# Kernel optimization log

Measured on AMD Instinct MI355X. Metric: run time of the kernel, lower is better.

The kernel has to match this reference:

```python
import jax, jax.numpy as jnp
import numpy as np

N_EMBD = 1024
B, T = 4, 2048

def setup_inputs() -> dict:
    key = jax.random.key(0)
    k1, k2, k3, k4 = jax.random.split(key, 4)
    s = 1.0 / np.sqrt(N_EMBD)
    return {
        "x": jax.random.normal(k1, (B, T, N_EMBD), dtype=jnp.float32),
        "Wq": jax.random.normal(k2, (N_EMBD, N_EMBD), dtype=jnp.float32) * s,
        "Wk": jax.random.normal(k3, (N_EMBD, N_EMBD), dtype=jnp.float32) * s,
        "Wv": jax.random.normal(k4, (N_EMBD, N_EMBD), dtype=jnp.float32) * s,
    }

def reference(x, Wq, Wk, Wv):
    # x: [B,T,C]; torch Linear (no bias): y = x @ W.T
    Bq, Tq, C = x.shape
    q = jnp.einsum('btc,dc->btd', x, Wq)
    k = jnp.einsum('btc,dc->btd', x, Wk)
    v = jnp.einsum('btc,dc->btd', x, Wv)
    att = jnp.einsum('bqd,bkd->bqk', q, k) / jnp.sqrt(jnp.float32(C))
    causal = jnp.tril(jnp.ones((Tq, Tq), dtype=bool))  # [T,T]
    att = jnp.where(causal, att, -jnp.inf)
    w = jax.nn.softmax(att, axis=-1)
    # dropout is identity in eval mode
    out = jnp.einsum('bqk,bkd->bqd', w, v)
    return out
```

## Files before the change

kernel.cpp:

```cpp
#include <hip/hip_runtime.h>
#include <stdint.h>

typedef __attribute__((ext_vector_type(8))) __bf16 bf16x8;
typedef __attribute__((ext_vector_type(8))) unsigned short ushort8;
typedef __attribute__((ext_vector_type(4))) float f32x4;

static __device__ __forceinline__ unsigned short f2bf(float f) {
  unsigned u = __float_as_uint(f);
  u += 0x7fffu + ((u >> 16) & 1u);
  return (unsigned short)(u >> 16);
}

union U16cast { ushort8 u; bf16x8 b; };
static __device__ __forceinline__ bf16x8 as_bf16x8(ushort8 x) { U16cast t; t.u = x; return t.b; }
static __device__ __forceinline__ bf16x8 ldfrag(const unsigned short* p) {
  return as_bf16x8(*(const ushort8*)p);
}

#define GLD_LDS16(g, l)                                                        \
  __builtin_amdgcn_global_load_lds(                                            \
      (const __attribute__((address_space(1))) void*)(g),                      \
      (__attribute__((address_space(3))) void*)(l), 16, 0, 0)

__global__ __launch_bounds__(256) void cast_all(
    const float* __restrict__ x, const float* __restrict__ Wq,
    const float* __restrict__ Wk, const float* __restrict__ Wv,
    unsigned short* __restrict__ out, float* __restrict__ lzero,
    long nx4, long nw4, long n4) {
  long g = (long)blockIdx.x * blockDim.x + threadIdx.x;
  if (g < 2048) ((float4*)lzero)[g] = (float4){0.f, 0.f, 0.f, 0.f};
  long i = g;
  long stride = (long)gridDim.x * blockDim.x;
  for (; i < n4; i += stride) {
    const float4* src;
    long j = i;
    if (j < nx4) {
      src = (const float4*)x;
    } else {
      j -= nx4;
      if (j < nw4) src = (const float4*)Wq;
      else if (j < 2 * nw4) { src = (const float4*)Wk; j -= nw4; }
      else { src = (const float4*)Wv; j -= 2 * nw4; }
    }
    float4 v = src[j];
    ushort4 o;
    o.x = f2bf(v.x); o.y = f2bf(v.y); o.z = f2bf(v.z); o.w = f2bf(v.w);
    *(ushort4*)(out + i * 4) = o;
  }
}

__global__ __launch_bounds__(512, 4) void gemm_qkv(
    const unsigned short* __restrict__ A, const unsigned short* __restrict__ B,
    unsigned short* __restrict__ qkv, unsigned short* __restrict__ vT) {
  __shared__ __align__(16) unsigned short As[3][4096];
  __shared__ __align__(16) unsigned short Bs[3][8192];

  int wg = blockIdx.x;
  wg = (wg & 7) * 96 + (wg >> 3);
  const int bm = wg / 12, bn = wg % 12;
  const int m0 = bm << 7, n0 = bn << 8;

  const int tid = threadIdx.x;

  const int srow = tid >> 2;
  const int sseg = (tid & 3) ^ ((srow >> 1) & 3);
  const unsigned short* sa = A + (long)(m0 + srow) * 1024 + sseg * 8;
  const unsigned short* sb0 = B + (long)(n0 + srow) * 1024 + sseg * 8;
  const unsigned short* sb1 = sb0 + (long)128 * 1024;
  unsigned short* dA = &As[0][0] + tid * 8;
  unsigned short* dB = &Bs[0][0] + tid * 8;

#define STG_SA(kt, s)  GLD_LDS16(sa + (kt) * 32, dA + (s) * 4096)
#define STG_SB0(kt, s) GLD_LDS16(sb0 + (kt) * 32, dB + (s) * 8192)
#define STG_SB1(kt, s) GLD_LDS16(sb1 + (kt) * 32, dB + (s) * 8192 + 4096)

  const int lane = tid & 63;
  const int w = tid >> 6;
  const int wr = w >> 2;
  const int wc = w & 3;
  const int fr = lane & 15;
  const int kb = lane >> 4;
  const int segr = (kb ^ ((fr >> 1) & 3)) << 3;
  const unsigned short* rA = &As[0][0] + (wr * 64 + fr) * 32 + segr;
  const unsigned short* rB = &Bs[0][0] + (wc * 64 + fr) * 32 + segr;

  f32x4 acc[4][4];
#pragma unroll
  for (int mf = 0; mf < 4; ++mf)
#pragma unroll
    for (int nf = 0; nf < 4; ++nf)
      acc[mf][nf] = (f32x4){0.f, 0.f, 0.f, 0.f};

  STG_SA(0, 0); STG_SB0(0, 0); STG_SB1(0, 0);
  STG_SA(1, 1); STG_SB0(1, 1); STG_SB1(1, 1);
  asm volatile("s_waitcnt vmcnt(3)" ::: "memory");
  __builtin_amdgcn_s_barrier();
  __builtin_amdgcn_sched_barrier(0);

  int c0 = 0, c2 = 2;
#pragma unroll 1
  for (int kt = 0; kt < 32; ++kt) {
    const unsigned short* pA = rA + c0 * 4096;
    const unsigned short* pB = rB + c0 * 8192;
    bf16x8 av[4], bv0, bv1, bv2, bv3;

#pragma unroll
    for (int mf = 0; mf < 4; ++mf) av[mf] = ldfrag(pA + mf * 512);
    bv0 = ldfrag(pB);
    bv1 = ldfrag(pB + 512);
    if (kt < 30) {
      STG_SA(kt + 2, c2);
      STG_SB0(kt + 2, c2);
      asm volatile("s_waitcnt vmcnt(3)" ::: "memory");
    } else {
      asm volatile("s_waitcnt vmcnt(0)" ::: "memory");
    }
    __builtin_amdgcn_s_barrier();
    asm volatile("s_waitcnt lgkmcnt(0)" ::: "memory");
    __builtin_amdgcn_sched_barrier(0);
    __builtin_amdgcn_s_setprio(1);
#pragma unroll
    for (int mf = 0; mf < 4; ++mf) {
      acc[mf][0] = __builtin_amdgcn_mfma_f32_16x16x32_bf16(av[mf], bv0, acc[mf][0], 0, 0, 0);
      acc[mf][1] = __builtin_amdgcn_mfma_f32_16x16x32_bf16(av[mf], bv1, acc[mf][1], 0, 0, 0);
    }
    __builtin_amdgcn_s_setprio(0);
    __builtin_amdgcn_s_barrier();
    __builtin_amdgcn_sched_barrier(0);

    bv2 = ldfrag(pB + 1024);
    bv3 = ldfrag(pB + 1536);
    if (kt < 30) {
      STG_SB1(kt + 2, c2);
      asm volatile("s_waitcnt vmcnt(3)" ::: "memory");
    } else {
      asm volatile("s_waitcnt vmcnt(0)" ::: "memory");
    }
    __builtin_amdgcn_s_barrier();
    asm volatile("s_waitcnt lgkmcnt(0)" ::: "memory");
    __builtin_amdgcn_sched_barrier(0);
    __builtin_amdgcn_s_setprio(1);
#pragma unroll
    for (int mf = 0; mf < 4; ++mf) {
      acc[mf][2] = __builtin_amdgcn_mfma_f32_16x16x32_bf16(av[mf], bv2, acc[mf][2], 0, 0, 0);
      acc[mf][3] = __builtin_amdgcn_mfma_f32_16x16x32_bf16(av[mf], bv3, acc[mf][3], 0, 0, 0);
    }
    __builtin_amdgcn_s_setprio(0);
    __builtin_amdgcn_s_barrier();
    __builtin_amdgcn_sched_barrier(0);

    c0 = (c0 == 2) ? 0 : c0 + 1;
    c2 = (c2 == 2) ? 0 : c2 + 1;
  }
#undef STG_SA
#undef STG_SB0
#undef STG_SB1

  const int rq = kb << 2;
  if (n0 < 2048) {
#pragma unroll
    for (int mf = 0; mf < 4; ++mf) {
      const int row = m0 + wr * 64 + mf * 16 + rq;
#pragma unroll
      for (int nf = 0; nf < 4; ++nf) {
        const int col = n0 + wc * 64 + nf * 16 + fr;
#pragma unroll
        for (int r = 0; r < 4; ++r)
          qkv[(long)(row + r) * 3072 + col] = f2bf(acc[mf][nf][r]);
      }
    }
  } else {
    const int b2 = m0 >> 11;
    const int t0 = (m0 & 2047) + wr * 64;
#pragma unroll
    for (int mf = 0; mf < 4; ++mf) {
      const int trow = t0 + mf * 16 + rq;
#pragma unroll
      for (int nf = 0; nf < 4; ++nf) {
        const int colv = (n0 - 2048) + wc * 64 + nf * 16 + fr;
        ushort4 o;
        o.x = f2bf(acc[mf][nf][0]); o.y = f2bf(acc[mf][nf][1]);
        o.z = f2bf(acc[mf][nf][2]); o.w = f2bf(acc[mf][nf][3]);
        *(ushort4*)(vT + ((long)b2 * 1024 + colv) * 2048 + trow) = o;
      }
    }
  }
}

template <int MODE>
__global__ __launch_bounds__(256, 4) void gemm128(
    const unsigned short* __restrict__ A, const unsigned short* __restrict__ Bp,
    void* __restrict__ Cout, float* __restrict__ lbuf) {
  __shared__ __align__(16) unsigned short As[2][4096];
  __shared__ __align__(16) unsigned short Bs[2][4096];

  constexpr int LDA = (MODE == 1) ? 3072 : 2048;

  const int wgid = blockIdx.x;
  int m0, n0, b;
  if constexpr (MODE == 1) {
    b = wgid & 3;
    const int t = wgid >> 2;
    int bm = 0;
    while ((bm + 2) * (bm + 1) / 2 <= t) ++bm;
    const int bn = t - bm * (bm + 1) / 2;
    m0 = bm << 7; n0 = bn << 7;
  } else {
    const int xcd = wgid & 7;
    const int inner = wgid >> 3;
    const int s = inner >> 5;
    const int rem = inner & 31;
    b = rem >> 3;
    const int bn = rem & 7;
    const int bm = s ? (15 - xcd) : xcd;
    m0 = bm << 7; n0 = bn << 7;
  }

  const unsigned short* Ab = A;
  const unsigned short* Bb = Bp;
  if constexpr (MODE == 1) {
    Ab += (long)b * 2048 * 3072;
    Bb += (long)b * 2048 * 3072;
  } else {
    Ab += (long)b * 2048 * 2048;
    Bb += (long)b * 1024 * 2048;
  }

  const int tid = threadIdx.x;

  const int srow = tid >> 2;
  const int sseg = (tid & 3) ^ ((srow >> 1) & 3);
  const unsigned short* sa = Ab + (long)(m0 + srow) * LDA + sseg * 8;
  const unsigned short* sb = Bb + (long)(n0 + srow) * LDA + sseg * 8;
  const long sRj = (long)64 * LDA;
  unsigned short* dA = &As[0][0] + tid * 8;
  unsigned short* dB = &Bs[0][0] + tid * 8;

#define STG(kt, s)                                                             \
  do {                                                                         \
    GLD_LDS16(sa + (kt) * 32, dA + (s) * 4096);                                \
    GLD_LDS16(sa + sRj + (kt) * 32, dA + (s) * 4096 + 2048);                   \
    GLD_LDS16(sb + (kt) * 32, dB + (s) * 4096);                                \
    GLD_LDS16(sb + sRj + (kt) * 32, dB + (s) * 4096 + 2048);                   \
  } while (0)

  const int lane = tid & 63;
  const int w = tid >> 6;
  const int wr = w >> 1;
  const int wc = w & 1;
  const int fr = lane & 15;
  const int kb = lane >> 4;
  const unsigned short* rA0 = &As[0][0] + wr * 64 * 32;
  const unsigned short* rB0 = &Bs[0][0] + wc * 64 * 32;

  f32x4 acc[4][4];
#pragma unroll
  for (int mf = 0; mf < 4; ++mf)
#pragma unroll
    for (int nf = 0; nf < 4; ++nf)
      acc[mf][nf] = (f32x4){0.f, 0.f, 0.f, 0.f};

  const int kend = (MODE == 2) ? (m0 + 128) : 1024;
  const int NT = kend >> 5;

  STG(0, 0);
  __syncthreads();

  for (int kt = 0; kt < NT; ++kt) {
    const int s = kt & 1;
    if (kt + 1 < NT) STG(kt + 1, s ^ 1);

    bf16x8 av[4], bvv[4];
#pragma unroll
    for (int mf = 0; mf < 4; ++mf) {
      const int row = mf * 16 + fr;
      const int segr = (kb ^ ((row >> 1) & 3)) << 3;
      av[mf] = ldfrag(rA0 + s * 4096 + row * 32 + segr);
    }
#pragma unroll
    for (int nf = 0; nf < 4; ++nf) {
      const int row = nf * 16 + fr;
      const int segr = (kb ^ ((row >> 1) & 3)) << 3;
      bvv[nf] = ldfrag(rB0 + s * 4096 + row * 32 + segr);
    }

#pragma unroll
    for (int mf = 0; mf < 4; ++mf)
#pragma unroll
      for (int nf = 0; nf < 4; ++nf)
        acc[mf][nf] = __builtin_amdgcn_mfma_f32_16x16x32_bf16(av[mf], bvv[nf], acc[mf][nf], 0, 0, 0);

    __syncthreads();
  }
#undef STG

  const int rq = kb << 2;
  if constexpr (MODE == 1) {
    unsigned short* Pu = (unsigned short*)Cout + (long)b * 2048 * 2048;
    float* lrow = lbuf + b * 2048;
#pragma unroll
    for (int mf = 0; mf < 4; ++mf) {
      const int row = m0 + wr * 64 + mf * 16 + rq;
      float psum0 = 0.f, psum1 = 0.f, psum2 = 0.f, psum3 = 0.f;
#pragma unroll
      for (int nf = 0; nf < 4; ++nf) {
        const int col = n0 + wc * 64 + nf * 16 + fr;
        float e0 = (col > row + 0) ? 0.f : __expf(acc[mf][nf][0] * 0.03125f);
        float e1 = (col > row + 1) ? 0.f : __expf(acc[mf][nf][1] * 0.03125f);
        float e2 = (col > row + 2) ? 0.f : __expf(acc[mf][nf][2] * 0.03125f);
        float e3 = (col > row + 3) ? 0.f : __expf(acc[mf][nf][3] * 0.03125f);
        psum0 += e0; psum1 += e1; psum2 += e2; psum3 += e3;
        Pu[(long)(row + 0) * 2048 + col] = f2bf(e0);
        Pu[(long)(row + 1) * 2048 + col] = f2bf(e1);
        Pu[(long)(row + 2) * 2048 + col] = f2bf(e2);
        Pu[(long)(row + 3) * 2048 + col] = f2bf(e3);
      }
#pragma unroll
      for (int off = 1; off < 16; off <<= 1) {
        psum0 += __shfl_xor(psum0, off);
        psum1 += __shfl_xor(psum1, off);
        psum2 += __shfl_xor(psum2, off);
        psum3 += __shfl_xor(psum3, off);
      }
      if (fr == 0) {
        atomicAdd(&lrow[row + 0], psum0);
        atomicAdd(&lrow[row + 1], psum1);
        atomicAdd(&lrow[row + 2], psum2);
        atomicAdd(&lrow[row + 3], psum3);
      }
    }
  } else {
    float* Cf = (float*)Cout + (long)b * 2048 * 1024;
    const float* lrow = lbuf + b * 2048;
#pragma unroll
    for (int mf = 0; mf < 4; ++mf) {
      const int row = m0 + wr * 64 + mf * 16 + rq;
      float il0 = 1.0f / lrow[row + 0];
      float il1 = 1.0f / lrow[row + 1];
      float il2 = 1.0f / lrow[row + 2];
      float il3 = 1.0f / lrow[row + 3];
#pragma unroll
      for (int nf = 0; nf < 4; ++nf) {
        const int col = n0 + wc * 64 + nf * 16 + fr;
        Cf[(long)(row + 0) * 1024 + col] = acc[mf][nf][0] * il0;
        Cf[(long)(row + 1) * 1024 + col] = acc[mf][nf][1] * il1;
        Cf[(long)(row + 2) * 1024 + col] = acc[mf][nf][2] * il2;
        Cf[(long)(row + 3) * 1024 + col] = acc[mf][nf][3] * il3;
      }
    }
  }
}

extern "C" void kernel_launch(void* const* d_in, const int* in_sizes, int n_in,
                              void* d_out, int out_size, void* d_ws, size_t ws_size,
                              hipStream_t stream) {
  const float* x  = (const float*)d_in[0];
  const float* Wq = (const float*)d_in[1];
  const float* Wk = (const float*)d_in[2];
  const float* Wv = (const float*)d_in[3];
  float* out = (float*)d_out;

  const int Bb = 4, T = 2048, C = 1024;
  const long BT = (long)Bb * T;
  const int N3 = 3 * C;

  char* ws = (char*)d_ws;
  unsigned short* xb   = (unsigned short*)ws; ws += BT * C * 2;
  unsigned short* wbuf = (unsigned short*)ws; ws += (long)N3 * C * 2;
  unsigned short* qkv  = (unsigned short*)ws; ws += BT * N3 * 2;
  unsigned short* vT   = (unsigned short*)ws; ws += BT * C * 2;
  unsigned short* Pu   = (unsigned short*)ws; ws += (long)Bb * T * T * 2;
  float* lbuf          = (float*)ws;          ws += BT * 4;

  const long nx4 = BT * C / 4, nw4 = (long)C * C / 4;
  cast_all<<<2048, 256, 0, stream>>>(x, Wq, Wk, Wv, xb, lbuf, nx4, nw4, nx4 + 3 * nw4);

  gemm_qkv<<<dim3(768, 1, 1), 512, 0, stream>>>(xb, wbuf, qkv, vT);

  gemm128<1><<<dim3(544, 1, 1), 256, 0, stream>>>(qkv, qkv + C, Pu, lbuf);

  gemm128<2><<<dim3(512, 1, 1), 256, 0, stream>>>(Pu, vT, out, lbuf);
}
```

Before: 157.5 us.

## Enlarge QKV GEMM tile to 256x256 with BK=64 double-buffered pipeline

The QKV projection GEMM now uses 256x256 output tiles with a K-step of 64 instead of 128x256 tiles with K-step 32, and a two-stage double buffer replaces the three-stage buffer. Each of the eight waves computes a 128x64 subtile in four interleaved phases, issuing global-to-LDS loads between MFMA phases. The grid is halved and the block swizzle is updated. The aim is more reuse per loaded byte and fewer barriers per FLOP. The cost is more LDS and registers, so occupancy drops to two blocks per CU, and 384 blocks leave a partial wave on the CUs.

```diff
diff --git a/kernel.cpp b/kernel.cpp
--- a/kernel.cpp
+++ b/kernel.cpp
@@ -16,6 +16,8 @@
 static __device__ __forceinline__ bf16x8 ldfrag(const unsigned short* p) {
   return as_bf16x8(*(const ushort8*)p);
 }
+
+#define MFMA16(a, b, c) __builtin_amdgcn_mfma_f32_16x16x32_bf16((a), (b), (c), 0, 0, 0)
 
 #define GLD_LDS16(g, l)                                                        \
   __builtin_amdgcn_global_load_lds(                                            \
@@ -49,30 +51,27 @@
   }
 }
 
-__global__ __launch_bounds__(512, 4) void gemm_qkv(
+__global__ __launch_bounds__(512, 2) void gemm_qkv(
     const unsigned short* __restrict__ A, const unsigned short* __restrict__ B,
     unsigned short* __restrict__ qkv, unsigned short* __restrict__ vT) {
-  __shared__ __align__(16) unsigned short As[3][4096];
-  __shared__ __align__(16) unsigned short Bs[3][8192];
+  __shared__ __align__(16) unsigned short As[2][16384];
+  __shared__ __align__(16) unsigned short Bs[2][16384];
 
   int wg = blockIdx.x;
-  wg = (wg & 7) * 96 + (wg >> 3);
+  wg = (wg & 7) * 48 + (wg >> 3);
   const int bm = wg / 12, bn = wg % 12;
-  const int m0 = bm << 7, n0 = bn << 8;
+  const int m0 = bm << 8, n0 = bn << 8;
 
   const int tid = threadIdx.x;
-
-  const int srow = tid >> 2;
-  const int sseg = (tid & 3) ^ ((srow >> 1) & 3);
-  const unsigned short* sa = A + (long)(m0 + srow) * 1024 + sseg * 8;
-  const unsigned short* sb0 = B + (long)(n0 + srow) * 1024 + sseg * 8;
-  const unsigned short* sb1 = sb0 + (long)128 * 1024;
-  unsigned short* dA = &As[0][0] + tid * 8;
-  unsigned short* dB = &Bs[0][0] + tid * 8;
-
-#define STG_SA(kt, s)  GLD_LDS16(sa + (kt) * 32, dA + (s) * 4096)
-#define STG_SB0(kt, s) GLD_LDS16(sb0 + (kt) * 32, dB + (s) * 8192)
-#define STG_SB1(kt, s) GLD_LDS16(sb1 + (kt) * 32, dB + (s) * 8192 + 4096)
+  const int sq = tid >> 3;
+  const int gseg = (tid & 7) ^ (sq & 7);
+  const unsigned short* pAg = A + (long)(m0 + sq) * 1024 + gseg * 8;
+  const unsigned short* pBg = B + (long)(n0 + sq) * 1024 + gseg * 8;
+  unsigned short* dAl = &As[0][0] + tid * 8;
+  unsigned short* dBl = &Bs[0][0] + tid * 8;
+
+#define SA(q, kt, bo) GLD_LDS16(pAg + (q) * 65536 + (kt) * 64, dAl + (bo) + (q) * 4096)
+#define SB(q, kt, bo) GLD_LDS16(pBg + (q) * 65536 + (kt) * 64, dBl + (bo) + (q) * 4096)
 
   const int lane = tid & 63;
   const int w = tid >> 6;
@@ -80,107 +79,147 @@
   const int wc = w & 3;
   const int fr = lane & 15;
   const int kb = lane >> 4;
-  const int segr = (kb ^ ((fr >> 1) & 3)) << 3;
-  const unsigned short* rA = &As[0][0] + (wr * 64 + fr) * 32 + segr;
-  const unsigned short* rB = &Bs[0][0] + (wc * 64 + fr) * 32 + segr;
-
-  f32x4 acc[4][4];
-#pragma unroll
-  for (int mf = 0; mf < 4; ++mf)
+  const int f7 = fr & 7;
+  const int s0 = (kb ^ f7) << 3;
+  const int s1 = s0 ^ 32;
+  const unsigned short* rA = &As[0][0] + (wr * 128 + fr) * 64;
+  const unsigned short* rB = &Bs[0][0] + (wc * 64 + fr) * 64;
+
+  f32x4 acc[8][4];
+#pragma unroll
+  for (int mf = 0; mf < 8; ++mf)
 #pragma unroll
     for (int nf = 0; nf < 4; ++nf)
       acc[mf][nf] = (f32x4){0.f, 0.f, 0.f, 0.f};
 
-  STG_SA(0, 0); STG_SB0(0, 0); STG_SB1(0, 0);
-  STG_SA(1, 1); STG_SB0(1, 1); STG_SB1(1, 1);
-  asm volatile("s_waitcnt vmcnt(3)" ::: "memory");
-  __builtin_amdgcn_s_barrier();
-  __builtin_amdgcn_sched_barrier(0);
-
-  int c0 = 0, c2 = 2;
+  bf16x8 av[4][2], b0[2][2], b1[2][2];
+
+  SB(0, 0, 0); SB(1, 0, 0); SB(2, 0, 0); SB(3, 0, 0);
+  SA(0, 0, 0); SA(2, 0, 0); SA(1, 0, 0); SA(3, 0, 0);
+
 #pragma unroll 1
-  for (int kt = 0; kt < 32; ++kt) {
-    const unsigned short* pA = rA + c0 * 4096;
-    const unsigned short* pB = rB + c0 * 8192;
-    bf16x8 av[4], bv0, bv1, bv2, bv3;
-
-#pragma unroll
-    for (int mf = 0; mf < 4; ++mf) av[mf] = ldfrag(pA + mf * 512);
-    bv0 = ldfrag(pB);
-    bv1 = ldfrag(pB + 512);
-    if (kt < 30) {
-      STG_SA(kt + 2, c2);
-      STG_SB0(kt + 2, c2);
-      asm volatile("s_waitcnt vmcnt(3)" ::: "memory");
-    } else {
-      asm volatile("s_waitcnt vmcnt(0)" ::: "memory");
-    }
-    __builtin_amdgcn_s_barrier();
+  for (int t = 0; t < 16; ++t) {
+    const int bo = (t & 1) << 14;
+    const int bo1 = bo ^ 16384;
+    const int k1 = t + 1;
+    const bool nl = (t < 15);
+    const unsigned short* pa = rA + bo;
+    const unsigned short* pb = rB + bo;
+
+    if (nl) { SB(0, k1, bo1); SB(1, k1, bo1); }
+    if (nl) asm volatile("s_waitcnt vmcnt(4)" ::: "memory");
+    else    asm volatile("s_waitcnt vmcnt(2)" ::: "memory");
+    __builtin_amdgcn_s_barrier();
+    __builtin_amdgcn_sched_barrier(0);
+#pragma unroll
+    for (int mf = 0; mf < 4; ++mf) {
+      av[mf][0] = ldfrag(pa + mf * 1024 + s0);
+      av[mf][1] = ldfrag(pa + mf * 1024 + s1);
+    }
+#pragma unroll
+    for (int nf = 0; nf < 2; ++nf) {
+      b0[nf][0] = ldfrag(pb + nf * 1024 + s0);
+      b0[nf][1] = ldfrag(pb + nf * 1024 + s1);
+    }
     asm volatile("s_waitcnt lgkmcnt(0)" ::: "memory");
     __builtin_amdgcn_sched_barrier(0);
     __builtin_amdgcn_s_setprio(1);
 #pragma unroll
+    for (int mf = 0; mf < 4; ++mf)
+#pragma unroll
+      for (int nf = 0; nf < 2; ++nf) {
+        acc[mf][nf] = MFMA16(av[mf][0], b0[nf][0], acc[mf][nf]);
+        acc[mf][nf] = MFMA16(av[mf][1], b0[nf][1], acc[mf][nf]);
+      }
+    __builtin_amdgcn_s_setprio(0);
+    __builtin_amdgcn_s_barrier();
+
+    if (nl) { SB(2, k1, bo1); SB(3, k1, bo1); }
+    __builtin_amdgcn_s_barrier();
+    __builtin_amdgcn_sched_barrier(0);
+#pragma unroll
+    for (int nf = 0; nf < 2; ++nf) {
+      b1[nf][0] = ldfrag(pb + 2048 + nf * 1024 + s0);
+      b1[nf][1] = ldfrag(pb + 2048 + nf * 1024 + s1);
+    }
+    asm volatile("s_waitcnt lgkmcnt(0)" ::: "memory");
+    __builtin_amdgcn_sched_barrier(0);
+    __builtin_amdgcn_s_setprio(1);
+#pragma unroll
+    for (int mf = 0; mf < 4; ++mf)
+#pragma unroll
+      for (int nf = 0; nf < 2; ++nf) {
+        acc[mf][2 + nf] = MFMA16(av[mf][0], b1[nf][0], acc[mf][2 + nf]);
+        acc[mf][2 + nf] = MFMA16(av[mf][1], b1[nf][1], acc[mf][2 + nf]);
+      }
+    __builtin_amdgcn_s_setprio(0);
+    __builtin_amdgcn_s_barrier();
+
+    if (nl) { SA(0, k1, bo1); SA(2, k1, bo1); }
+    if (nl) asm volatile("s_waitcnt vmcnt(6)" ::: "memory");
+    else    asm volatile("s_waitcnt vmcnt(0)" ::: "memory");
+    __builtin_amdgcn_s_barrier();
+    __builtin_amdgcn_sched_barrier(0);
+#pragma unroll
     for (int mf = 0; mf < 4; ++mf) {
-      acc[mf][0] = __builtin_amdgcn_mfma_f32_16x16x32_bf16(av[mf], bv0, acc[mf][0], 0, 0, 0);
-      acc[mf][1] = __builtin_amdgcn_mfma_f32_16x16x32_bf16(av[mf], bv1, acc[mf][1], 0, 0, 0);
-    }
+      av[mf][0] = ldfrag(pa + 4096 + mf * 1024 + s0);
+      av[mf][1] = ldfrag(pa + 4096 + mf * 1024 + s1);
+    }
+    asm volatile("s_waitcnt lgkmcnt(0)" ::: "memory");
+    __builtin_amdgcn_sched_barrier(0);
+    __builtin_amdgcn_s_setprio(1);
+#pragma unroll
+    for (int mf = 0; mf < 4; ++mf)
+#pragma unroll
+      for (int nf = 0; nf < 2; ++nf) {
+        acc[4 + mf][nf] = MFMA16(av[mf][0], b0[nf][0], acc[4 + mf][nf]);
+        acc[4 + mf][nf] = MFMA16(av[mf][1], b0[nf][1], acc[4 + mf][nf]);
+      }
     __builtin_amdgcn_s_setprio(0);
     __builtin_amdgcn_s_barrier();
-    __builtin_amdgcn_sched_barrier(0);
-
-    bv2 = ldfrag(pB + 1024);
-    bv3 = ldfrag(pB + 1536);
-    if (kt < 30) {
-      STG_SB1(kt + 2, c2);
-      asm volatile("s_waitcnt vmcnt(3)" ::: "memory");
-    } else {
-      asm volatile("s_waitcnt vmcnt(0)" ::: "memory");
-    }
-    __builtin_amdgcn_s_barrier();
-    asm volatile("s_waitcnt lgkmcnt(0)" ::: "memory");
+
+    if (nl) { SA(1, k1, bo1); SA(3, k1, bo1); }
+    __builtin_amdgcn_s_barrier();
     __builtin_amdgcn_sched_barrier(0);
     __builtin_amdgcn_s_setprio(1);
 #pragma unroll
-    for (int mf = 0; mf < 4; ++mf) {
-      acc[mf][2] = __builtin_amdgcn_mfma_f32_16x16x32_bf16(av[mf], bv2, acc[mf][2], 0, 0, 0);
-      acc[mf][3] = __builtin_amdgcn_mfma_f32_16x16x32_bf16(av[mf], bv3, acc[mf][3], 0, 0, 0);
-    }
+    for (int mf = 0; mf < 4; ++mf)
+#pragma unroll
+      for (int nf = 0; nf < 2; ++nf) {
+        acc[4 + mf][2 + nf] = MFMA16(av[mf][0], b1[nf][0], acc[4 + mf][2 + nf]);
+        acc[4 + mf][2 + nf] = MFMA16(av[mf][1], b1[nf][1], acc[4 + mf][2 + nf]);
+      }
     __builtin_amdgcn_s_setprio(0);
     __builtin_amdgcn_s_barrier();
-    __builtin_amdgcn_sched_barrier(0);
-
-    c0 = (c0 == 2) ? 0 : c0 + 1;
-    c2 = (c2 == 2) ? 0 : c2 + 1;
-  }
-#undef STG_SA
-#undef STG_SB0
-#undef STG_SB1
+  }
+#undef SA
+#undef SB
 
   const int rq = kb << 2;
   if (n0 < 2048) {
 #pragma unroll
-    for (int mf = 0; mf < 4; ++mf) {
-      const int row = m0 + wr * 64 + mf * 16 + rq;
-#pragma unroll
-      for (int nf = 0; nf < 4; ++nf) {
-        const int col = n0 + wc * 64 + nf * 16 + fr;
+    for (int mfg = 0; mfg < 8; ++mfg) {
+      const int row = m0 + wr * 128 + mfg * 16 + rq;
+#pragma unroll
+      for (int nfg = 0; nfg < 4; ++nfg) {
+        const int col = n0 + wc * 64 + nfg * 16 + fr;
 #pragma unroll
         for (int r = 0; r < 4; ++r)
-          qkv[(long)(row + r) * 3072 + col] = f2bf(acc[mf][nf][r]);
+          qkv[(long)(row + r) * 3072 + col] = f2bf(acc[mfg][nfg][r]);
       }
     }
   } else {
     const int b2 = m0 >> 11;
-    const int t0 = (m0 & 2047) + wr * 64;
-#pragma unroll
-    for (int mf = 0; mf < 4; ++mf) {
-      const int trow = t0 + mf * 16 + rq;
-#pragma unroll
-      for (int nf = 0; nf < 4; ++nf) {
-        const int colv = (n0 - 2048) + wc * 64 + nf * 16 + fr;
+    const int t0v = (m0 & 2047) + wr * 128;
+#pragma unroll
+    for (int mfg = 0; mfg < 8; ++mfg) {
+      const int trow = t0v + mfg * 16 + rq;
+#pragma unroll
+      for (int nfg = 0; nfg < 4; ++nfg) {
+        const int colv = (n0 - 2048) + wc * 64 + nfg * 16 + fr;
         ushort4 o;
-        o.x = f2bf(acc[mf][nf][0]); o.y = f2bf(acc[mf][nf][1]);
-        o.z = f2bf(acc[mf][nf][2]); o.w = f2bf(acc[mf][nf][3]);
+        o.x = f2bf(acc[mfg][nfg][0]); o.y = f2bf(acc[mfg][nfg][1]);
+        o.z = f2bf(acc[mfg][nfg][2]); o.w = f2bf(acc[mfg][nfg][3]);
         *(ushort4*)(vT + ((long)b2 * 1024 + colv) * 2048 + trow) = o;
       }
     }
@@ -288,7 +327,7 @@
     for (int mf = 0; mf < 4; ++mf)
 #pragma unroll
       for (int nf = 0; nf < 4; ++nf)
-        acc[mf][nf] = __builtin_amdgcn_mfma_f32_16x16x32_bf16(av[mf], bvv[nf], acc[mf][nf], 0, 0, 0);
+        acc[mf][nf] = MFMA16(av[mf], bvv[nf], acc[mf][nf]);
 
     __syncthreads();
   }
@@ -375,7 +414,7 @@
   const long nx4 = BT * C / 4, nw4 = (long)C * C / 4;
   cast_all<<<2048, 256, 0, stream>>>(x, Wq, Wk, Wv, xb, lbuf, nx4, nw4, nx4 + 3 * nw4);
 
-  gemm_qkv<<<dim3(768, 1, 1), 512, 0, stream>>>(xb, wbuf, qkv, vT);
+  gemm_qkv<<<dim3(384, 1, 1), 512, 0, stream>>>(xb, wbuf, qkv, vT);
 
   gemm128<1><<<dim3(544, 1, 1), 256, 0, stream>>>(qkv, qkv + C, Pu, lbuf);
 
```

Measured after the change: 185.0 us. 1.17x slower.
